# Optimization experiments

Measured on AMD Instinct MI355X. Metric: run time of the kernel, lower is better.

Reference implementation:

```python
import jax, jax.numpy as jnp
import numpy as np

N_NODES = 50000
N_EDGES = 800000
IN_FEATS = 64
OUT_FEATS = 64
EDGE_DIM = 8


def setup_inputs() -> dict:
    key = jax.random.key(0)
    k1, k2, k3, k4, k5 = jax.random.split(key, 5)
    node_feat = jax.random.normal(k1, (N_NODES, IN_FEATS), dtype=jnp.float32)
    edge_feat = jax.random.normal(k2, (N_EDGES, EDGE_DIM), dtype=jnp.float32)
    W = jax.random.normal(k3, (OUT_FEATS, IN_FEATS), dtype=jnp.float32) * (1.0 / np.sqrt(IN_FEATS))
    b = jnp.zeros((OUT_FEATS,), dtype=jnp.float32)
    src = jax.random.randint(k4, (N_EDGES,), 0, N_NODES, dtype=jnp.int64 if jax.config.jax_enable_x64 else jnp.int32)
    dst = jax.random.randint(k5, (N_EDGES,), 0, N_NODES, dtype=jnp.int64 if jax.config.jax_enable_x64 else jnp.int32)
    return {"node_feat": node_feat, "edge_feat": edge_feat, "W": W, "b": b,
            "src": src, "dst": dst}


def reference(node_feat, edge_feat, W, b, src, dst):
    # EfConv forward with aggregate='sum', node_feat.shape[1] == in_feats.
    n_nodes = node_feat.shape[0]
    edge_dim = edge_feat.shape[1]
    h_src = node_feat[src]  # [E, in_feats] gather once, reused for every slice
    aggs = []
    for k in range(edge_dim):  # small fixed loop over edge feature slices
        m = h_src * edge_feat[:, k:k + 1]                      # u_mul_e: [E, in_feats]
        aggs.append(jax.ops.segment_sum(m, dst, num_segments=n_nodes))
    agg = jnp.stack(aggs, axis=1)                              # [N, edge_dim, in_feats]
    # per-slice shared linear, then concat along feature dim
    out = jnp.einsum('nki,oi->nko', agg, W) + b                # [N, edge_dim, out_feats]
    return out.reshape(n_nodes, edge_dim * W.shape[0])         # [N, edge_dim*out_feats]
```

## Files before the change

### kernel.cpp

```cpp
#include <hip/hip_runtime.h>


#define FEATS 64
#define EDGE_DIM 8

__global__ void __launch_bounds__(256) transform_kernel(
    const float* __restrict__ nf, const float* __restrict__ W,
    float* __restrict__ t, int n_nodes)
{
    __shared__ float sWt[FEATS * 65];
    __shared__ float srow[4][FEATS];
    const int tid = threadIdx.x;

    #pragma unroll
    for (int base = 0; base < FEATS * FEATS; base += 256) {
        int idx = base + tid;
        int o = idx >> 6;
        int i = idx & 63;
        sWt[i * 65 + o] = W[idx];
    }

    const int r = tid >> 6;
    const int o = tid & 63;
    const int node = blockIdx.x * 4 + r;
    if (node < n_nodes) srow[r][o] = nf[(long)node * FEATS + o];
    __syncthreads();

    if (node >= n_nodes) return;
    float sum = 0.f;
    #pragma unroll
    for (int i = 0; i < FEATS; i++)
        sum += srow[r][i] * sWt[i * 65 + o];
    t[(long)node * FEATS + o] = sum;
}

__global__ void __launch_bounds__(256) zero_kernel(int* __restrict__ p, int n)
{
    int i = blockIdx.x * 256 + threadIdx.x;
    if (i < n) p[i] = 0;
}

__global__ void __launch_bounds__(256) hist_kernel(
    const int* __restrict__ dst, int* __restrict__ deg, int n_edges)
{
    int e = blockIdx.x * 256 + threadIdx.x;
    if (e < n_edges) atomicAdd(&deg[dst[e]], 1);
}

__global__ void __launch_bounds__(256) partials_kernel(
    const int* __restrict__ deg, int* __restrict__ partials, int n)
{
    __shared__ int s[256];
    int i = blockIdx.x * 256 + threadIdx.x;
    s[threadIdx.x] = (i < n) ? deg[i] : 0;
    __syncthreads();
    for (int off = 128; off > 0; off >>= 1) {
        if (threadIdx.x < off) s[threadIdx.x] += s[threadIdx.x + off];
        __syncthreads();
    }
    if (threadIdx.x == 0) partials[blockIdx.x] = s[0];
}

__global__ void __launch_bounds__(256) scan_partials_kernel(
    const int* __restrict__ partials, int* __restrict__ pscan, int nb)
{
    __shared__ int s[256];
    int tid = threadIdx.x;
    s[tid] = (tid < nb) ? partials[tid] : 0;
    for (int off = 1; off < 256; off <<= 1) {
        __syncthreads();
        int x = (tid >= off) ? s[tid - off] : 0;
        __syncthreads();
        s[tid] += x;
    }
    __syncthreads();
    pscan[tid] = (tid == 0) ? 0 : s[tid - 1];
}

__global__ void __launch_bounds__(256) scan_addback_kernel(
    const int* __restrict__ deg, const int* __restrict__ pscan,
    int* __restrict__ offsets, int* __restrict__ cursor,
    int n, int n_edges)
{
    __shared__ int s[256];
    int tid = threadIdx.x;
    int i = blockIdx.x * 256 + tid;
    int v = (i < n) ? deg[i] : 0;
    s[tid] = v;
    for (int off = 1; off < 256; off <<= 1) {
        __syncthreads();
        int x = (tid >= off) ? s[tid - off] : 0;
        __syncthreads();
        s[tid] += x;
    }
    __syncthreads();
    if (i < n) {
        int excl = pscan[blockIdx.x] + s[tid] - v;
        offsets[i] = excl;
        cursor[i]  = excl;
    }
    if (blockIdx.x == 0 && tid == 0) offsets[n] = n_edges;
}

__global__ void __launch_bounds__(256) permute_kernel(
    const int* __restrict__ src, const int* __restrict__ dst,
    int* __restrict__ cursor, int* __restrict__ src_s, int* __restrict__ perm,
    int n_edges)
{
    int e = blockIdx.x * 256 + threadIdx.x;
    if (e >= n_edges) return;
    int pos = atomicAdd(&cursor[dst[e]], 1);
    src_s[pos] = src[e];
    perm[pos] = e;
}

__global__ void __launch_bounds__(256) aggregate_kernel(
    const float* __restrict__ t, const float* __restrict__ ef,
    const int* __restrict__ src_s, const int* __restrict__ perm,
    const int* __restrict__ offsets, const float* __restrict__ b,
    float* __restrict__ out, int n_nodes)
{
    int node = (blockIdx.x * 256 + threadIdx.x) >> 6;
    int o = threadIdx.x & 63;
    if (node >= n_nodes) return;

    int beg = offsets[node];
    int end = offsets[node + 1];
    float acc[EDGE_DIM];
    #pragma unroll
    for (int k = 0; k < EDGE_DIM; k++) acc[k] = 0.f;

    int j = beg;
    for (; j + 1 < end; j += 2) {
        int e0 = perm[j],     e1 = perm[j + 1];
        int s0 = src_s[j],    s1 = src_s[j + 1];
        float tv0 = t[(long)s0 * FEATS + o];
        float tv1 = t[(long)s1 * FEATS + o];
        const float4* p0 = (const float4*)(ef + (long)e0 * EDGE_DIM);
        const float4* p1 = (const float4*)(ef + (long)e1 * EDGE_DIM);
        float4 a0 = p0[0], a1 = p0[1];
        float4 c0 = p1[0], c1 = p1[1];
        acc[0] += a0.x * tv0; acc[1] += a0.y * tv0;
        acc[2] += a0.z * tv0; acc[3] += a0.w * tv0;
        acc[4] += a1.x * tv0; acc[5] += a1.y * tv0;
        acc[6] += a1.z * tv0; acc[7] += a1.w * tv0;
        acc[0] += c0.x * tv1; acc[1] += c0.y * tv1;
        acc[2] += c0.z * tv1; acc[3] += c0.w * tv1;
        acc[4] += c1.x * tv1; acc[5] += c1.y * tv1;
        acc[6] += c1.z * tv1; acc[7] += c1.w * tv1;
    }
    if (j < end) {
        int e0 = perm[j];
        int s0 = src_s[j];
        float tv0 = t[(long)s0 * FEATS + o];
        const float4* p0 = (const float4*)(ef + (long)e0 * EDGE_DIM);
        float4 a0 = p0[0], a1 = p0[1];
        acc[0] += a0.x * tv0; acc[1] += a0.y * tv0;
        acc[2] += a0.z * tv0; acc[3] += a0.w * tv0;
        acc[4] += a1.x * tv0; acc[5] += a1.y * tv0;
        acc[6] += a1.z * tv0; acc[7] += a1.w * tv0;
    }

    float bo = b[o];
    float* op = out + (long)node * (EDGE_DIM * FEATS) + o;
    #pragma unroll
    for (int k = 0; k < EDGE_DIM; k++)
        op[k * FEATS] = acc[k] + bo;
}

extern "C" void kernel_launch(void* const* d_in, const int* in_sizes, int n_in,
                              void* d_out, int out_size, void* d_ws, size_t ws_size,
                              hipStream_t stream) {
    const float* node_feat = (const float*)d_in[0];
    const float* edge_feat = (const float*)d_in[1];
    const float* W         = (const float*)d_in[2];
    const float* b         = (const float*)d_in[3];
    const int*   src       = (const int*)d_in[4];
    const int*   dst       = (const int*)d_in[5];
    float* out = (float*)d_out;

    const int n_nodes = in_sizes[0] / FEATS;
    const int n_edges = in_sizes[4];
    const int nb_nodes = (n_nodes + 255) / 256;
    const int nb_edges = (n_edges + 255) / 256;

    int* w = (int*)d_ws;
    float* t      = (float*)w;
    int* deg      = w + (long)n_nodes * FEATS;
    int* offsets  = deg + n_nodes;
    int* cursor   = offsets + n_nodes + 1;
    int* partials = cursor + n_nodes;
    int* pscan    = partials + 256;
    int* src_s    = pscan + 256;
    int* perm     = src_s + n_edges;

    transform_kernel<<<(n_nodes + 3) / 4, 256, 0, stream>>>(node_feat, W, t, n_nodes);
    zero_kernel<<<nb_nodes, 256, 0, stream>>>(deg, n_nodes);
    hist_kernel<<<nb_edges, 256, 0, stream>>>(dst, deg, n_edges);
    partials_kernel<<<nb_nodes, 256, 0, stream>>>(deg, partials, n_nodes);
    scan_partials_kernel<<<1, 256, 0, stream>>>(partials, pscan, nb_nodes);
    scan_addback_kernel<<<nb_nodes, 256, 0, stream>>>(deg, pscan, offsets, cursor,
                                                      n_nodes, n_edges);
    permute_kernel<<<nb_edges, 256, 0, stream>>>(src, dst, cursor, src_s, perm, n_edges);

    const long total_ag = (long)n_nodes * 64;
    aggregate_kernel<<<(int)((total_ag + 255) / 256), 256, 0, stream>>>(
        t, edge_feat, src_s, perm, offsets, b, out, n_nodes);
}
```

Baseline: 333.1 us.

## Pre-permute edge features into CSR order and stream them in aggregation

The permute step now scatters edge features into destination-sorted order, so the aggregation kernel reads them contiguously instead of doing random gathers through a perm array. The deg zeroing moves into the transform kernel, which removes one launch. The histogram kernel handles four edges per thread with int4 loads, and output stores become nontemporal. In exchange the scatter writes 25.6MB of extra workspace, and the fast path is only taken when the workspace is large enough and the pointers are aligned.

```diff
diff --git a/kernel.cpp b/kernel.cpp
--- a/kernel.cpp
+++ b/kernel.cpp
@@ -6,7 +6,7 @@
 
 __global__ void __launch_bounds__(256) transform_kernel(
     const float* __restrict__ nf, const float* __restrict__ W,
-    float* __restrict__ t, int n_nodes)
+    float* __restrict__ t, int* __restrict__ deg, int n_nodes)
 {
     __shared__ float sWt[FEATS * 65];
     __shared__ float srow[4][FEATS];
@@ -15,15 +15,17 @@
     #pragma unroll
     for (int base = 0; base < FEATS * FEATS; base += 256) {
         int idx = base + tid;
-        int o = idx >> 6;
-        int i = idx & 63;
-        sWt[i * 65 + o] = W[idx];
+        sWt[(idx & 63) * 65 + (idx >> 6)] = W[idx];
     }
 
     const int r = tid >> 6;
     const int o = tid & 63;
     const int node = blockIdx.x * 4 + r;
     if (node < n_nodes) srow[r][o] = nf[(long)node * FEATS + o];
+    if (tid < 4) {
+        int zn = blockIdx.x * 4 + tid;
+        if (zn < n_nodes) deg[zn] = 0;
+    }
     __syncthreads();
 
     if (node >= n_nodes) return;
@@ -34,17 +36,19 @@
     t[(long)node * FEATS + o] = sum;
 }
 
-__global__ void __launch_bounds__(256) zero_kernel(int* __restrict__ p, int n)
-{
-    int i = blockIdx.x * 256 + threadIdx.x;
-    if (i < n) p[i] = 0;
-}
-
 __global__ void __launch_bounds__(256) hist_kernel(
     const int* __restrict__ dst, int* __restrict__ deg, int n_edges)
 {
-    int e = blockIdx.x * 256 + threadIdx.x;
-    if (e < n_edges) atomicAdd(&deg[dst[e]], 1);
+    int i = (blockIdx.x * 256 + threadIdx.x) * 4;
+    if (i + 3 < n_edges) {
+        int4 d = *(const int4*)(dst + i);
+        atomicAdd(&deg[d.x], 1);
+        atomicAdd(&deg[d.y], 1);
+        atomicAdd(&deg[d.z], 1);
+        atomicAdd(&deg[d.w], 1);
+    } else {
+        for (int e = i; e < n_edges; e++) atomicAdd(&deg[dst[e]], 1);
+    }
 }
 
 __global__ void __launch_bounds__(256) partials_kernel(
@@ -102,6 +106,20 @@
     if (blockIdx.x == 0 && tid == 0) offsets[n] = n_edges;
 }
 
+__global__ void __launch_bounds__(256) permute_ef_kernel(
+    const int* __restrict__ src, const int* __restrict__ dst,
+    const float4* __restrict__ ef4, int* __restrict__ cursor,
+    int* __restrict__ src_s, float4* __restrict__ efs4, int n_edges)
+{
+    int e = blockIdx.x * 256 + threadIdx.x;
+    if (e >= n_edges) return;
+    int pos = atomicAdd(&cursor[dst[e]], 1);
+    src_s[pos] = src[e];
+    float4 a = ef4[2l * e], c = ef4[2l * e + 1];
+    efs4[2l * pos] = a;
+    efs4[2l * pos + 1] = c;
+}
+
 __global__ void __launch_bounds__(256) permute_kernel(
     const int* __restrict__ src, const int* __restrict__ dst,
     int* __restrict__ cursor, int* __restrict__ src_s, int* __restrict__ perm,
@@ -114,6 +132,59 @@
     perm[pos] = e;
 }
 
+__global__ void __launch_bounds__(256) aggregate_stream_kernel(
+    const float* __restrict__ t, const float4* __restrict__ efs4,
+    const int* __restrict__ src_s, const int* __restrict__ offsets,
+    const float* __restrict__ b, float* __restrict__ out, int n_nodes)
+{
+    int node = (blockIdx.x * 256 + threadIdx.x) >> 6;
+    int o = threadIdx.x & 63;
+    if (node >= n_nodes) return;
+
+    int beg = offsets[node];
+    int end = offsets[node + 1];
+    float acc[EDGE_DIM];
+    #pragma unroll
+    for (int k = 0; k < EDGE_DIM; k++) acc[k] = 0.f;
+
+    int j = beg;
+    for (; j + 3 < end; j += 4) {
+        int s0 = src_s[j],     s1 = src_s[j + 1];
+        int s2 = src_s[j + 2], s3 = src_s[j + 3];
+        float tv0 = t[(long)s0 * FEATS + o];
+        float tv1 = t[(long)s1 * FEATS + o];
+        float tv2 = t[(long)s2 * FEATS + o];
+        float tv3 = t[(long)s3 * FEATS + o];
+        float4 a0 = efs4[2l * j],     a1 = efs4[2l * j + 1];
+        float4 b0 = efs4[2l * j + 2], b1 = efs4[2l * j + 3];
+        float4 c0 = efs4[2l * j + 4], c1 = efs4[2l * j + 5];
+        float4 d0 = efs4[2l * j + 6], d1 = efs4[2l * j + 7];
+        acc[0] += a0.x * tv0 + b0.x * tv1 + c0.x * tv2 + d0.x * tv3;
+        acc[1] += a0.y * tv0 + b0.y * tv1 + c0.y * tv2 + d0.y * tv3;
+        acc[2] += a0.z * tv0 + b0.z * tv1 + c0.z * tv2 + d0.z * tv3;
+        acc[3] += a0.w * tv0 + b0.w * tv1 + c0.w * tv2 + d0.w * tv3;
+        acc[4] += a1.x * tv0 + b1.x * tv1 + c1.x * tv2 + d1.x * tv3;
+        acc[5] += a1.y * tv0 + b1.y * tv1 + c1.y * tv2 + d1.y * tv3;
+        acc[6] += a1.z * tv0 + b1.z * tv1 + c1.z * tv2 + d1.z * tv3;
+        acc[7] += a1.w * tv0 + b1.w * tv1 + c1.w * tv2 + d1.w * tv3;
+    }
+    for (; j < end; j++) {
+        int s0 = src_s[j];
+        float tv0 = t[(long)s0 * FEATS + o];
+        float4 a0 = efs4[2l * j], a1 = efs4[2l * j + 1];
+        acc[0] += a0.x * tv0; acc[1] += a0.y * tv0;
+        acc[2] += a0.z * tv0; acc[3] += a0.w * tv0;
+        acc[4] += a1.x * tv0; acc[5] += a1.y * tv0;
+        acc[6] += a1.z * tv0; acc[7] += a1.w * tv0;
+    }
+
+    float bo = b[o];
+    float* op = out + (long)node * (EDGE_DIM * FEATS) + o;
+    #pragma unroll
+    for (int k = 0; k < EDGE_DIM; k++)
+        __builtin_nontemporal_store(acc[k] + bo, op + k * FEATS);
+}
+
 __global__ void __launch_bounds__(256) aggregate_kernel(
     const float* __restrict__ t, const float* __restrict__ ef,
     const int* __restrict__ src_s, const int* __restrict__ perm,
@@ -132,22 +203,22 @@
 
     int j = beg;
     for (; j + 1 < end; j += 2) {
-        int e0 = perm[j],     e1 = perm[j + 1];
-        int s0 = src_s[j],    s1 = src_s[j + 1];
+        int e0 = perm[j], e1 = perm[j + 1];
+        int s0 = src_s[j], s1 = src_s[j + 1];
         float tv0 = t[(long)s0 * FEATS + o];
         float tv1 = t[(long)s1 * FEATS + o];
         const float4* p0 = (const float4*)(ef + (long)e0 * EDGE_DIM);
         const float4* p1 = (const float4*)(ef + (long)e1 * EDGE_DIM);
         float4 a0 = p0[0], a1 = p0[1];
         float4 c0 = p1[0], c1 = p1[1];
-        acc[0] += a0.x * tv0; acc[1] += a0.y * tv0;
-        acc[2] += a0.z * tv0; acc[3] += a0.w * tv0;
-        acc[4] += a1.x * tv0; acc[5] += a1.y * tv0;
-        acc[6] += a1.z * tv0; acc[7] += a1.w * tv0;
-        acc[0] += c0.x * tv1; acc[1] += c0.y * tv1;
-        acc[2] += c0.z * tv1; acc[3] += c0.w * tv1;
-        acc[4] += c1.x * tv1; acc[5] += c1.y * tv1;
-        acc[6] += c1.z * tv1; acc[7] += c1.w * tv1;
+        acc[0] += a0.x * tv0 + c0.x * tv1;
+        acc[1] += a0.y * tv0 + c0.y * tv1;
+        acc[2] += a0.z * tv0 + c0.z * tv1;
+        acc[3] += a0.w * tv0 + c0.w * tv1;
+        acc[4] += a1.x * tv0 + c1.x * tv1;
+        acc[5] += a1.y * tv0 + c1.y * tv1;
+        acc[6] += a1.z * tv0 + c1.z * tv1;
+        acc[7] += a1.w * tv0 + c1.w * tv1;
     }
     if (j < end) {
         int e0 = perm[j];
@@ -165,7 +236,7 @@
     float* op = out + (long)node * (EDGE_DIM * FEATS) + o;
     #pragma unroll
     for (int k = 0; k < EDGE_DIM; k++)
-        op[k * FEATS] = acc[k] + bo;
+        __builtin_nontemporal_store(acc[k] + bo, op + k * FEATS);
 }
 
 extern "C" void kernel_launch(void* const* d_in, const int* in_sizes, int n_in,
@@ -192,18 +263,29 @@
     int* partials = cursor + n_nodes;
     int* pscan    = partials + 256;
     int* src_s    = pscan + 256;
-    int* perm     = src_s + n_edges;
-
-    transform_kernel<<<(n_nodes + 3) / 4, 256, 0, stream>>>(node_feat, W, t, n_nodes);
-    zero_kernel<<<nb_nodes, 256, 0, stream>>>(deg, n_nodes);
-    hist_kernel<<<nb_edges, 256, 0, stream>>>(dst, deg, n_edges);
+    int* tail     = src_s + n_edges;
+
+    const size_t need_efs = ((size_t)(tail - w) + (size_t)n_edges * EDGE_DIM) * 4;
+    const bool use_efs = (ws_size >= need_efs) &&
+                         ((((uintptr_t)edge_feat) & 15) == 0) &&
+                         ((((uintptr_t)tail) & 15) == 0);
+
+    transform_kernel<<<(n_nodes + 3) / 4, 256, 0, stream>>>(node_feat, W, t, deg, n_nodes);
+    hist_kernel<<<(n_edges + 1023) / 1024, 256, 0, stream>>>(dst, deg, n_edges);
     partials_kernel<<<nb_nodes, 256, 0, stream>>>(deg, partials, n_nodes);
     scan_partials_kernel<<<1, 256, 0, stream>>>(partials, pscan, nb_nodes);
     scan_addback_kernel<<<nb_nodes, 256, 0, stream>>>(deg, pscan, offsets, cursor,
                                                       n_nodes, n_edges);
-    permute_kernel<<<nb_edges, 256, 0, stream>>>(src, dst, cursor, src_s, perm, n_edges);
 
     const long total_ag = (long)n_nodes * 64;
-    aggregate_kernel<<<(int)((total_ag + 255) / 256), 256, 0, stream>>>(
-        t, edge_feat, src_s, perm, offsets, b, out, n_nodes);
-}
+    if (use_efs) {
+        permute_ef_kernel<<<nb_edges, 256, 0, stream>>>(
+            src, dst, (const float4*)edge_feat, cursor, src_s, (float4*)tail, n_edges);
+        aggregate_stream_kernel<<<(int)((total_ag + 255) / 256), 256, 0, stream>>>(
+            t, (const float4*)tail, src_s, offsets, b, out, n_nodes);
+    } else {
+        permute_kernel<<<nb_edges, 256, 0, stream>>>(src, dst, cursor, src_s, tail, n_edges);
+        aggregate_kernel<<<(int)((total_ag + 255) / 256), 256, 0, stream>>>(
+            t, edge_feat, src_s, tail, offsets, b, out, n_nodes);
+    }
+}
```

New measurement: 333.3 us. No clear change (+0.1%).
